# Kernel optimization log

Hardware: AMD Instinct MI355X
Metric: run time of the kernel (lower is better)

## Reference

```python
import jax, jax.numpy as jnp
import numpy as np

N_BINS = 15


def setup_inputs() -> dict:
    key = jax.random.key(0)
    k1, k2 = jax.random.split(key)
    N, C = 2_000_000, 100
    logits = jax.random.normal(k1, (N, C), dtype=jnp.float32)
    labels = jax.random.randint(k2, (N,), 0, C, dtype=jnp.int64)
    temperature = jnp.ones((1,), dtype=jnp.float32)
    return {"logits": logits, "labels": labels, "temperature": temperature}


def reference(logits, labels, temperature):
    # logits: [N, C], labels: [N] int, temperature: [1]
    softmaxes = jax.nn.softmax(logits / temperature[0], axis=1)
    confidences = jnp.max(softmaxes, axis=1)            # [N]
    predictions = jnp.argmax(softmaxes, axis=1)          # [N]
    accuracies = (predictions == labels).astype(softmaxes.dtype)

    # bin b covers (b/n_bins, (b+1)/n_bins]; ceil(conf*n)-1 gives exactly that
    # half-open-on-left binning (conf > 0 always holds after softmax).
    bin_idx = jnp.clip(
        jnp.ceil(confidences * N_BINS).astype(jnp.int32) - 1, 0, N_BINS - 1
    )

    ones = jnp.ones_like(confidences)
    counts = jax.ops.segment_sum(ones, bin_idx, num_segments=N_BINS)
    sum_conf = jax.ops.segment_sum(confidences, bin_idx, num_segments=N_BINS)
    sum_acc = jax.ops.segment_sum(accuracies, bin_idx, num_segments=N_BINS)

    n_total = confidences.shape[0]
    prop_in_bin = counts / n_total
    safe_counts = jnp.maximum(counts, 1.0)
    avg_conf = sum_conf / safe_counts
    avg_acc = sum_acc / safe_counts
    gap = jnp.where(counts > 0, jnp.abs(avg_conf - avg_acc), 0.0)
    ece = jnp.sum(gap * prop_in_bin)
    return ece.reshape(1)
```

## Files before the change

kernel.cpp:

```cpp
#include <hip/hip_runtime.h>
#include <math.h>

#define NBINS 15

__global__ void ece_init(float* accum) {
    int t = threadIdx.x;
    if (t < 48) accum[t] = 0.0f;
}

__global__ __launch_bounds__(256) void ece_main(
    const float* __restrict__ logits,
    const int* __restrict__ labels,
    const float* __restrict__ temp,
    float* __restrict__ accum,
    int N)
{
    const float invT = 1.0f / temp[0];
    const int tid  = threadIdx.x;
    const int lane = tid & 63;
    const int c    = lane & 15;
    const int g    = lane >> 4;
    const int wavesPerBlock = blockDim.x >> 6;
    const long long waveId     = (long long)blockIdx.x * wavesPerBlock + (tid >> 6);
    const long long totalWaves = (long long)gridDim.x * wavesPerBlock;

    float cnt = 0.f, sconf = 0.f, sacc = 0.f;
    const bool has2 = (c < 9);

    for (long long base = waveId * 4; base < (long long)N; base += totalWaves * 4) {
        long long row = base + g;
        const bool valid = (row < (long long)N);
        const long long r = valid ? row : (long long)(N - 1);
        const float* rowp = logits + (size_t)r * 100;

        float4 a = *reinterpret_cast<const float4*>(rowp + 4 * c);
        float4 b;
        if (has2) {
            b = *reinterpret_cast<const float4*>(rowp + 64 + 4 * c);
        } else {
            b = make_float4(-INFINITY, -INFINITY, -INFINITY, -INFINITY);
        }
        a.x *= invT; a.y *= invT; a.z *= invT; a.w *= invT;
        b.x *= invT; b.y *= invT; b.z *= invT; b.w *= invT;

        float lm = a.x; int lidx = 4 * c;
        if (a.y > lm) { lm = a.y; lidx = 4 * c + 1; }
        if (a.z > lm) { lm = a.z; lidx = 4 * c + 2; }
        if (a.w > lm) { lm = a.w; lidx = 4 * c + 3; }
        if (b.x > lm) { lm = b.x; lidx = 64 + 4 * c; }
        if (b.y > lm) { lm = b.y; lidx = 64 + 4 * c + 1; }
        if (b.z > lm) { lm = b.z; lidx = 64 + 4 * c + 2; }
        if (b.w > lm) { lm = b.w; lidx = 64 + 4 * c + 3; }

        float gm = lm;
        gm = fmaxf(gm, __shfl_xor(gm, 1));
        gm = fmaxf(gm, __shfl_xor(gm, 2));
        gm = fmaxf(gm, __shfl_xor(gm, 4));
        gm = fmaxf(gm, __shfl_xor(gm, 8));

        int cand = (lm == gm) ? lidx : 0x7fffffff;
        cand = min(cand, __shfl_xor(cand, 1));
        cand = min(cand, __shfl_xor(cand, 2));
        cand = min(cand, __shfl_xor(cand, 4));
        cand = min(cand, __shfl_xor(cand, 8));

        float s = __expf(a.x - gm) + __expf(a.y - gm)
                + __expf(a.z - gm) + __expf(a.w - gm);
        if (has2) {
            s += __expf(b.x - gm) + __expf(b.y - gm)
               + __expf(b.z - gm) + __expf(b.w - gm);
        }
        s += __shfl_xor(s, 1);
        s += __shfl_xor(s, 2);
        s += __shfl_xor(s, 4);
        s += __shfl_xor(s, 8);

        float conf = 1.0f / s;
        int  lbl  = labels[r];
        float acc = (cand == lbl) ? 1.0f : 0.0f;
        int bin = (int)ceilf(conf * 15.0f) - 1;
        bin = bin < 0 ? 0 : (bin > 14 ? 14 : bin);

        if (valid && c == bin) {
            cnt   += 1.0f;
            sconf += conf;
            sacc  += acc;
        }
    }

    __shared__ float sh[48];
    if (tid < 48) sh[tid] = 0.0f;
    __syncthreads();
    if (c < NBINS) {
        atomicAdd(&sh[c],      cnt);
        atomicAdd(&sh[16 + c], sconf);
        atomicAdd(&sh[32 + c], sacc);
    }
    __syncthreads();
    if (tid < 48) {
        atomicAdd(&accum[tid], sh[tid]);
    }
}

__global__ void ece_final(const float* __restrict__ accum, float* __restrict__ out, float nTotal) {
    if (threadIdx.x == 0) {
        float e = 0.0f;
        for (int b = 0; b < NBINS; b++) {
            float cntv = accum[b];
            float sc   = accum[16 + b];
            float sa   = accum[32 + b];
            float safe = fmaxf(cntv, 1.0f);
            float gap  = (cntv > 0.0f) ? fabsf(sc / safe - sa / safe) : 0.0f;
            e += gap * (cntv / nTotal);
        }
        out[0] = e;
    }
}

extern "C" void kernel_launch(void* const* d_in, const int* in_sizes, int n_in,
                              void* d_out, int out_size, void* d_ws, size_t ws_size,
                              hipStream_t stream) {
    const float* logits = (const float*)d_in[0];
    const int*   labels = (const int*)d_in[1];
    const float* temp   = (const float*)d_in[2];
    float* accum = (float*)d_ws;
    const int N = in_sizes[1];

    ece_init<<<1, 64, 0, stream>>>(accum);
    ece_main<<<2048, 256, 0, stream>>>(logits, labels, temp, accum, N);
    ece_final<<<1, 64, 0, stream>>>(accum, (float*)d_out, (float)N);
}
```

Baseline: 175.7 us.

## Unroll ECE loop to 8 rows per wave with nontemporal loads and exp2 softmax

The main loop now handles two 4-row groups per iteration, giving more loads in flight per wave. Logit loads use nontemporal hints, and the temperature scale is folded with log2(e) so the raw exp2 hardware instruction can be used. Each lane computes its exponential sum against its own local max before the cross-lane max reduction, then rescales once by exp2(lm - gm), which takes the exp work off the dependency chain behind the shuffles. The cost is higher register pressure and slightly different floating-point rounding from the local-max rescaling.

New measurement: 174.1 us. About the same (-0.9%).

```diff
diff --git a/kernel.cpp b/kernel.cpp
--- a/kernel.cpp
+++ b/kernel.cpp
@@ -3,9 +3,74 @@
 
 #define NBINS 15
 
+typedef float f32x4 __attribute__((ext_vector_type(4)));
+
 __global__ void ece_init(float* accum) {
     int t = threadIdx.x;
     if (t < 48) accum[t] = 0.0f;
+}
+
+__device__ __forceinline__ void process4(
+    const f32x4* __restrict__ logits4,
+    const int* __restrict__ labels,
+    long long base, int g, int c, bool has2, float k, int N,
+    float& cnt, float& sconf, float& sacc)
+{
+    long long row = base + g;
+    const bool valid = (row < (long long)N);
+    const long long r = valid ? row : (long long)(N - 1);
+    const f32x4* rowp4 = logits4 + (size_t)r * 25;
+
+    f32x4 a = __builtin_nontemporal_load(rowp4 + c);
+    f32x4 b = (f32x4){-INFINITY, -INFINITY, -INFINITY, -INFINITY};
+    if (has2) b = __builtin_nontemporal_load(rowp4 + 16 + c);
+
+    a *= k;
+    b *= k;
+
+    float lm = a.x; int lidx = 4 * c;
+    if (a.y > lm) { lm = a.y; lidx = 4 * c + 1; }
+    if (a.z > lm) { lm = a.z; lidx = 4 * c + 2; }
+    if (a.w > lm) { lm = a.w; lidx = 4 * c + 3; }
+    if (b.x > lm) { lm = b.x; lidx = 64 + 4 * c; }
+    if (b.y > lm) { lm = b.y; lidx = 64 + 4 * c + 1; }
+    if (b.z > lm) { lm = b.z; lidx = 64 + 4 * c + 2; }
+    if (b.w > lm) { lm = b.w; lidx = 64 + 4 * c + 3; }
+
+    float s0 = __builtin_amdgcn_exp2f(a.x - lm) + __builtin_amdgcn_exp2f(a.y - lm)
+             + __builtin_amdgcn_exp2f(a.z - lm) + __builtin_amdgcn_exp2f(a.w - lm)
+             + __builtin_amdgcn_exp2f(b.x - lm) + __builtin_amdgcn_exp2f(b.y - lm)
+             + __builtin_amdgcn_exp2f(b.z - lm) + __builtin_amdgcn_exp2f(b.w - lm);
+
+    float gm = lm;
+    gm = fmaxf(gm, __shfl_xor(gm, 1));
+    gm = fmaxf(gm, __shfl_xor(gm, 2));
+    gm = fmaxf(gm, __shfl_xor(gm, 4));
+    gm = fmaxf(gm, __shfl_xor(gm, 8));
+
+    int cand = (lm == gm) ? lidx : 0x7fffffff;
+    cand = min(cand, __shfl_xor(cand, 1));
+    cand = min(cand, __shfl_xor(cand, 2));
+    cand = min(cand, __shfl_xor(cand, 4));
+    cand = min(cand, __shfl_xor(cand, 8));
+
+    float s = s0 * __builtin_amdgcn_exp2f(lm - gm);
+    s += __shfl_xor(s, 1);
+    s += __shfl_xor(s, 2);
+    s += __shfl_xor(s, 4);
+    s += __shfl_xor(s, 8);
+
+    float conf = 1.0f / s;
+    int   lbl  = labels[r];
+    float acc  = (cand == lbl) ? 1.0f : 0.0f;
+    int bin = (int)ceilf(conf * 15.0f) - 1;
+    bin = bin < 0 ? 0 : (bin > 14 ? 14 : bin);
+
+    if (valid && c == bin) {
+        cnt   += 1.0f;
+        sconf += conf;
+        sacc  += acc;
+    }
 }
 
 __global__ __launch_bounds__(256) void ece_main(
@@ -15,7 +80,7 @@
     float* __restrict__ accum,
     int N)
 {
-    const float invT = 1.0f / temp[0];
+    const float k = (1.0f / temp[0]) * 1.44269504088896340736f;
     const int tid  = threadIdx.x;
     const int lane = tid & 63;
     const int c    = lane & 15;
@@ -24,68 +89,13 @@
     const long long waveId     = (long long)blockIdx.x * wavesPerBlock + (tid >> 6);
     const long long totalWaves = (long long)gridDim.x * wavesPerBlock;
 
+    const f32x4* logits4 = reinterpret_cast<const f32x4*>(logits);
     float cnt = 0.f, sconf = 0.f, sacc = 0.f;
     const bool has2 = (c < 9);
 
-    for (long long base = waveId * 4; base < (long long)N; base += totalWaves * 4) {
-        long long row = base + g;
-        const bool valid = (row < (long long)N);
-        const long long r = valid ? row : (long long)(N - 1);
-        const float* rowp = logits + (size_t)r * 100;
-
-        float4 a = *reinterpret_cast<const float4*>(rowp + 4 * c);
-        float4 b;
-        if (has2) {
-            b = *reinterpret_cast<const float4*>(rowp + 64 + 4 * c);
-        } else {
-            b = make_float4(-INFINITY, -INFINITY, -INFINITY, -INFINITY);
-        }
-        a.x *= invT; a.y *= invT; a.z *= invT; a.w *= invT;
-        b.x *= invT; b.y *= invT; b.z *= invT; b.w *= invT;
-
-        float lm = a.x; int lidx = 4 * c;
-        if (a.y > lm) { lm = a.y; lidx = 4 * c + 1; }
-        if (a.z > lm) { lm = a.z; lidx = 4 * c + 2; }
-        if (a.w > lm) { lm = a.w; lidx = 4 * c + 3; }
-        if (b.x > lm) { lm = b.x; lidx = 64 + 4 * c; }
-        if (b.y > lm) { lm = b.y; lidx = 64 + 4 * c + 1; }
-        if (b.z > lm) { lm = b.z; lidx = 64 + 4 * c + 2; }
-        if (b.w > lm) { lm = b.w; lidx = 64 + 4 * c + 3; }
-
-        float gm = lm;
-        gm = fmaxf(gm, __shfl_xor(gm, 1));
-        gm = fmaxf(gm, __shfl_xor(gm, 2));
-        gm = fmaxf(gm, __shfl_xor(gm, 4));
-        gm = fmaxf(gm, __shfl_xor(gm, 8));
-
-        int cand = (lm == gm) ? lidx : 0x7fffffff;
-        cand = min(cand, __shfl_xor(cand, 1));
-        cand = min(cand, __shfl_xor(cand, 2));
-        cand = min(cand, __shfl_xor(cand, 4));
-        cand = min(cand, __shfl_xor(cand, 8));
-
-        float s = __expf(a.x - gm) + __expf(a.y - gm)
-                + __expf(a.z - gm) + __expf(a.w - gm);
-        if (has2) {
-            s += __expf(b.x - gm) + __expf(b.y - gm)
-               + __expf(b.z - gm) + __expf(b.w - gm);
-        }
-        s += __shfl_xor(s, 1);
-        s += __shfl_xor(s, 2);
-        s += __shfl_xor(s, 4);
-        s += __shfl_xor(s, 8);
-
-        float conf = 1.0f / s;
-        int  lbl  = labels[r];
-        float acc = (cand == lbl) ? 1.0f : 0.0f;
-        int bin = (int)ceilf(conf * 15.0f) - 1;
-        bin = bin < 0 ? 0 : (bin > 14 ? 14 : bin);
-
-        if (valid && c == bin) {
-            cnt   += 1.0f;
-            sconf += conf;
-            sacc  += acc;
-        }
+    for (long long base = waveId * 8; base < (long long)N; base += totalWaves * 8) {
+        process4(logits4, labels, base,     g, c, has2, k, N, cnt, sconf, sacc);
+        process4(logits4, labels, base + 4, g, c, has2, k, N, cnt, sconf, sacc);
     }
 
     __shared__ float sh[48];
```
